# Kernel tuning notes

Hardware: AMD Instinct MI355X
Metric: run time of the kernel (lower is better)

## Reference

```python
import jax, jax.numpy as jnp
import numpy as np

# Quantum kernel math: ansatz applies RY(x_d) then RY(-y_d) on wire d (wires independent),
# so state on wire d is RY(x_d - y_d)|0>, and amplitude of |00..0> is prod_d cos((x_d - y_d)/2).
# Kernel returns its absolute value: sim(x, y) = prod_d |cos((x_d - y_d)/2)|.

def setup_inputs() -> dict:
    key = jax.random.key(0)
    k1, k2, k3 = jax.random.split(key, 3)
    N, D = 4096, 4
    inputs = jax.random.normal(k1, (N, D), dtype=jnp.float32)
    rotation_params = jax.random.normal(k2, (D * D,), dtype=jnp.float32)
    entangle_params = jax.random.normal(k3, (D * D,), dtype=jnp.float32)
    return {"inputs": inputs, "rotation_params": rotation_params, "entangle_params": entangle_params}


def reference(inputs, rotation_params, entangle_params):
    D = inputs.shape[1]  # embed_dim = n_wires = 4
    q = inputs @ rotation_params.reshape(D, -1)   # [N, D]
    k = inputs @ entangle_params.reshape(D, -1)   # [N, D]
    v = inputs
    # Vectorized quantum kernel over all (i, j) pairs: [N, N, D] diff -> [N, N] sim
    diff = q[:, None, :] - k[None, :, :]
    sim = jnp.prod(jnp.abs(jnp.cos(diff * 0.5)), axis=-1)  # [N, N]
    scores = jax.nn.softmax(sim / jnp.sqrt(jnp.float32(D)), axis=-1)
    return scores @ v
```

## Files before the change

### kernel.cpp

```cpp
#include <hip/hip_runtime.h>

#define NROW 4096

__global__ __launch_bounds__(256) void qs_precompute_kernel(
    const float* __restrict__ inp, const float* __restrict__ rot,
    const float* __restrict__ ent, float* __restrict__ pre) {
  int r = blockIdx.x * 256 + threadIdx.x;
  if (r >= NROW) return;
  float4 x = reinterpret_cast<const float4*>(inp)[r];
  float cq[4], sq[4], ck[4], sk[4];
#pragma unroll
  for (int d = 0; d < 4; ++d) {
    float q = x.x * rot[0 * 4 + d] + x.y * rot[1 * 4 + d] +
              x.z * rot[2 * 4 + d] + x.w * rot[3 * 4 + d];
    float k = x.x * ent[0 * 4 + d] + x.y * ent[1 * 4 + d] +
              x.z * ent[2 * 4 + d] + x.w * ent[3 * 4 + d];
    __sincosf(0.5f * q, &sq[d], &cq[d]);
    __sincosf(0.5f * k, &sk[d], &ck[d]);
  }
  float4* p = reinterpret_cast<float4*>(pre + (size_t)r * 16);
  p[0] = make_float4(cq[0], cq[1], cq[2], cq[3]);
  p[1] = make_float4(sq[0], sq[1], sq[2], sq[3]);
  p[2] = make_float4(ck[0], ck[1], ck[2], ck[3]);
  p[3] = make_float4(sk[0], sk[1], sk[2], sk[3]);
}

__global__ __launch_bounds__(1024) void attn_kernel(
    const float* __restrict__ inp, const float* __restrict__ pre,
    float* __restrict__ out) {
  __shared__ float red[16][16][5];
  const int tid = threadIdx.x;
  const int wave = tid >> 6;
  const int lane = tid & 63;
  const int rloc = lane & 15;
  const int row = (blockIdx.x << 4) + rloc;
  const int slice = (wave << 2) + (lane >> 4);
  const int jbase = slice << 6;

  const float4* pr = reinterpret_cast<const float4*>(pre + (size_t)row * 16);
  const float4 cq = pr[0];
  const float4 sq = pr[1];

  float denom = 0.f, a0 = 0.f, a1 = 0.f, a2 = 0.f, a3 = 0.f;

#pragma unroll 4
  for (int it = 0; it < 64; ++it) {
    int j = jbase + it;
    const float4* pj = reinterpret_cast<const float4*>(pre + (size_t)j * 16);
    float4 ck = pj[2];
    float4 sk = pj[3];
    float4 v = reinterpret_cast<const float4*>(inp)[j];
    float t0 = fmaf(cq.x, ck.x, sq.x * sk.x);
    float t1 = fmaf(cq.y, ck.y, sq.y * sk.y);
    float t2 = fmaf(cq.z, ck.z, sq.z * sk.z);
    float t3 = fmaf(cq.w, ck.w, sq.w * sk.w);
    float sim = fabsf(t0 * t1 * t2 * t3);
    float e = __builtin_amdgcn_exp2f(sim * 0.72134752044448170367f);
    denom += e;
    a0 = fmaf(e, v.x, a0);
    a1 = fmaf(e, v.y, a1);
    a2 = fmaf(e, v.z, a2);
    a3 = fmaf(e, v.w, a3);
  }

#pragma unroll
  for (int off = 16; off <= 32; off <<= 1) {
    denom += __shfl_xor(denom, off, 64);
    a0 += __shfl_xor(a0, off, 64);
    a1 += __shfl_xor(a1, off, 64);
    a2 += __shfl_xor(a2, off, 64);
    a3 += __shfl_xor(a3, off, 64);
  }
  if (lane < 16) {
    red[wave][rloc][0] = denom;
    red[wave][rloc][1] = a0;
    red[wave][rloc][2] = a1;
    red[wave][rloc][3] = a2;
    red[wave][rloc][4] = a3;
  }
  __syncthreads();

  if (wave == 0) {
    const int grp = lane >> 4;
    float d = 0.f, b0 = 0.f, b1 = 0.f, b2 = 0.f, b3 = 0.f;
#pragma unroll
    for (int i = 0; i < 4; ++i) {
      const float* p = red[grp * 4 + i][rloc];
      d += p[0];
      b0 += p[1];
      b1 += p[2];
      b2 += p[3];
      b3 += p[4];
    }
#pragma unroll
    for (int off = 16; off <= 32; off <<= 1) {
      d += __shfl_xor(d, off, 64);
      b0 += __shfl_xor(b0, off, 64);
      b1 += __shfl_xor(b1, off, 64);
      b2 += __shfl_xor(b2, off, 64);
      b3 += __shfl_xor(b3, off, 64);
    }
    if (lane < 16) {
      reinterpret_cast<float4*>(out)[row] =
          make_float4(b0 / d, b1 / d, b2 / d, b3 / d);
    }
  }
}

extern "C" void kernel_launch(void* const* d_in, const int* in_sizes, int n_in,
                              void* d_out, int out_size, void* d_ws, size_t ws_size,
                              hipStream_t stream) {
  const float* inp = (const float*)d_in[0];
  const float* rot = (const float*)d_in[1];
  const float* ent = (const float*)d_in[2];
  float* out = (float*)d_out;
  float* pre = (float*)d_ws;

  qs_precompute_kernel<<<NROW / 256, 256, 0, stream>>>(inp, rot, ent, pre);
  attn_kernel<<<NROW / 16, 1024, 0, stream>>>(inp, pre, out);
}
```

Measured before the change: 82.41 us.

## Fuse precompute into attention kernel with per-block key trig staged in LDS

Result: faster. 68.41 us (-17.0%).

```diff
diff --git a/kernel.cpp b/kernel.cpp
--- a/kernel.cpp
+++ b/kernel.cpp
@@ -1,66 +1,86 @@
 #include <hip/hip_runtime.h>
 
+typedef float f2 __attribute__((ext_vector_type(2)));
+
 #define NROW 4096
+#define HJ   2048
 
-__global__ __launch_bounds__(256) void qs_precompute_kernel(
+__global__ __launch_bounds__(1024) void fused_attn_kernel(
     const float* __restrict__ inp, const float* __restrict__ rot,
-    const float* __restrict__ ent, float* __restrict__ pre) {
-  int r = blockIdx.x * 256 + threadIdx.x;
-  if (r >= NROW) return;
-  float4 x = reinterpret_cast<const float4*>(inp)[r];
-  float cq[4], sq[4], ck[4], sk[4];
-#pragma unroll
-  for (int d = 0; d < 4; ++d) {
-    float q = x.x * rot[0 * 4 + d] + x.y * rot[1 * 4 + d] +
-              x.z * rot[2 * 4 + d] + x.w * rot[3 * 4 + d];
-    float k = x.x * ent[0 * 4 + d] + x.y * ent[1 * 4 + d] +
-              x.z * ent[2 * 4 + d] + x.w * ent[3 * 4 + d];
-    __sincosf(0.5f * q, &sq[d], &cq[d]);
-    __sincosf(0.5f * k, &sk[d], &ck[d]);
-  }
-  float4* p = reinterpret_cast<float4*>(pre + (size_t)r * 16);
-  p[0] = make_float4(cq[0], cq[1], cq[2], cq[3]);
-  p[1] = make_float4(sq[0], sq[1], sq[2], sq[3]);
-  p[2] = make_float4(ck[0], ck[1], ck[2], ck[3]);
-  p[3] = make_float4(sk[0], sk[1], sk[2], sk[3]);
-}
-
-__global__ __launch_bounds__(1024) void attn_kernel(
-    const float* __restrict__ inp, const float* __restrict__ pre,
-    float* __restrict__ out) {
-  __shared__ float red[16][16][5];
-  const int tid = threadIdx.x;
+    const float* __restrict__ ent, float* __restrict__ out) {
+  __shared__ float4 kt[2 * HJ];
+  const int tid  = threadIdx.x;
   const int wave = tid >> 6;
   const int lane = tid & 63;
   const int rloc = lane & 15;
-  const int row = (blockIdx.x << 4) + rloc;
-  const int slice = (wave << 2) + (lane >> 4);
-  const int jbase = slice << 6;
+  const int row  = (blockIdx.x << 4) + rloc;
+  const int g    = (wave << 2) + (lane >> 4);
 
-  const float4* pr = reinterpret_cast<const float4*>(pre + (size_t)row * 16);
-  const float4 cq = pr[0];
-  const float4 sq = pr[1];
+  const float4* inp4 = reinterpret_cast<const float4*>(inp);
+
+  float4 xr = inp4[row];
+  float qc[4], qs[4];
+#pragma unroll
+  for (int d = 0; d < 4; ++d) {
+    float a = fmaf(xr.x, 0.5f * rot[d],
+              fmaf(xr.y, 0.5f * rot[4 + d],
+              fmaf(xr.z, 0.5f * rot[8 + d], xr.w * (0.5f * rot[12 + d]))));
+    __sincosf(a, &qs[d], &qc[d]);
+  }
+  f2 qc01 = {qc[0], qc[1]}, qc23 = {qc[2], qc[3]};
+  f2 qs01 = {qs[0], qs[1]}, qs23 = {qs[2], qs[3]};
+
+  const float phs = (tid & 1) ? -1.57079632679489662f : 0.f;
 
   float denom = 0.f, a0 = 0.f, a1 = 0.f, a2 = 0.f, a3 = 0.f;
 
+  for (int h = 0; h < 2; ++h) {
+    if (h) __syncthreads();
+#pragma unroll
+    for (int qq = 0; qq < 4; ++qq) {
+      int e = qq * 1024 + tid;
+      int j = e >> 1;
+      float4 xj = inp4[h * HJ + j];
+      float4 val;
+      val.x = __cosf(fmaf(xj.x, 0.5f * ent[0],
+                     fmaf(xj.y, 0.5f * ent[4],
+                     fmaf(xj.z, 0.5f * ent[8],
+                     fmaf(xj.w, 0.5f * ent[12], phs)))));
+      val.y = __cosf(fmaf(xj.x, 0.5f * ent[1],
+                     fmaf(xj.y, 0.5f * ent[5],
+                     fmaf(xj.z, 0.5f * ent[9],
+                     fmaf(xj.w, 0.5f * ent[13], phs)))));
+      val.z = __cosf(fmaf(xj.x, 0.5f * ent[2],
+                     fmaf(xj.y, 0.5f * ent[6],
+                     fmaf(xj.z, 0.5f * ent[10],
+                     fmaf(xj.w, 0.5f * ent[14], phs)))));
+      val.w = __cosf(fmaf(xj.x, 0.5f * ent[3],
+                     fmaf(xj.y, 0.5f * ent[7],
+                     fmaf(xj.z, 0.5f * ent[11],
+                     fmaf(xj.w, 0.5f * ent[15], phs)))));
+      kt[e] = val;
+    }
+    __syncthreads();
+
 #pragma unroll 4
-  for (int it = 0; it < 64; ++it) {
-    int j = jbase + it;
-    const float4* pj = reinterpret_cast<const float4*>(pre + (size_t)j * 16);
-    float4 ck = pj[2];
-    float4 sk = pj[3];
-    float4 v = reinterpret_cast<const float4*>(inp)[j];
-    float t0 = fmaf(cq.x, ck.x, sq.x * sk.x);
-    float t1 = fmaf(cq.y, ck.y, sq.y * sk.y);
-    float t2 = fmaf(cq.z, ck.z, sq.z * sk.z);
-    float t3 = fmaf(cq.w, ck.w, sq.w * sk.w);
-    float sim = fabsf(t0 * t1 * t2 * t3);
-    float e = __builtin_amdgcn_exp2f(sim * 0.72134752044448170367f);
-    denom += e;
-    a0 = fmaf(e, v.x, a0);
-    a1 = fmaf(e, v.y, a1);
-    a2 = fmaf(e, v.z, a2);
-    a3 = fmaf(e, v.w, a3);
+    for (int it = 0; it < 32; ++it) {
+      int jj = (it << 6) + g;
+      float4 c4 = kt[jj * 2];
+      float4 s4 = kt[jj * 2 + 1];
+      float4 v = inp4[h * HJ + jj];
+      f2 c01 = {c4.x, c4.y}, c23 = {c4.z, c4.w};
+      f2 s01 = {s4.x, s4.y}, s23 = {s4.z, s4.w};
+      f2 t01 = c01 * qc01 + s01 * qs01;
+      f2 t23 = c23 * qc23 + s23 * qs23;
+      f2 p = t01 * t23;
+      float m = p.x * p.y;
+      float e = __builtin_amdgcn_exp2f(fabsf(m) * 0.72134752044448170367f);
+      denom += e;
+      a0 = fmaf(e, v.x, a0);
+      a1 = fmaf(e, v.y, a1);
+      a2 = fmaf(e, v.z, a2);
+      a3 = fmaf(e, v.w, a3);
+    }
   }
 
 #pragma unroll
@@ -71,12 +91,16 @@
     a2 += __shfl_xor(a2, off, 64);
     a3 += __shfl_xor(a3, off, 64);
   }
+
+  __syncthreads();
+  float* red = reinterpret_cast<float*>(kt);
   if (lane < 16) {
-    red[wave][rloc][0] = denom;
-    red[wave][rloc][1] = a0;
-    red[wave][rloc][2] = a1;
-    red[wave][rloc][3] = a2;
-    red[wave][rloc][4] = a3;
+    int base = (wave * 16 + rloc) * 5;
+    red[base + 0] = denom;
+    red[base + 1] = a0;
+    red[base + 2] = a1;
+    red[base + 3] = a2;
+    red[base + 4] = a3;
   }
   __syncthreads();
 
@@ -85,7 +109,7 @@
     float d = 0.f, b0 = 0.f, b1 = 0.f, b2 = 0.f, b3 = 0.f;
 #pragma unroll
     for (int i = 0; i < 4; ++i) {
-      const float* p = red[grp * 4 + i][rloc];
+      const float* p = red + ((grp * 4 + i) * 16 + rloc) * 5;
       d += p[0];
       b0 += p[1];
       b1 += p[2];
@@ -114,8 +138,7 @@
   const float* rot = (const float*)d_in[1];
   const float* ent = (const float*)d_in[2];
   float* out = (float*)d_out;
-  float* pre = (float*)d_ws;
+  (void)d_ws; (void)ws_size;
 
-  qs_precompute_kernel<<<NROW / 256, 256, 0, stream>>>(inp, rot, ent, pre);
-  attn_kernel<<<NROW / 16, 1024, 0, stream>>>(inp, pre, out);
+  fused_attn_kernel<<<NROW / 16, 1024, 0, stream>>>(inp, rot, ent, out);
 }
```
